# Performance work log

Hardware: AMD Instinct MI355X
Metric: run time of the kernel (lower is better)

The kernel has to match this reference:

```python
import jax, jax.numpy as jnp
import numpy as np

B, N, D = 4, 10000, 64
C, E = 2, 160000  # adj channels, edges per (graph, channel)
EPS = 1e-10


def setup_inputs() -> dict:
    key = jax.random.key(0)
    k1, k2, k3 = jax.random.split(key, 3)
    inputs = jax.random.normal(k1, (B, N, D), dtype=jnp.float32)
    edge_idx = jax.random.randint(k2, (B, C, E, 2), 0, N, dtype=jnp.int32)
    weight_a = 0.1 * jax.random.normal(k3, (C, 2 * D, 1), dtype=jnp.float32)
    return {"inputs": inputs, "edge_idx": edge_idx, "weight_a": weight_a}


def _gat_channel(x, idx, wa):
    # x: [N, D], idx: [E, 2] (col 0 = scatter/dst node, col 1 = gather/src node), wa: [2D, 1]
    n = x.shape[0]
    a1 = x[idx[:, 1]]                      # [E, D]
    a2 = x[idx[:, 0]]                      # [E, D]
    score = jnp.concatenate([a1, a2], axis=1) @ wa   # [E, 1]
    e = jnp.exp(jax.nn.leaky_relu(score, negative_slope=0.2))  # [E, 1]
    denom = jax.ops.segment_sum(e, idx[:, 0], num_segments=n)  # [N, 1]  (ii @ e)
    denom_e = denom[idx[:, 1]]             # [E, 1]  (faithful to original: gather by idx[:,1])
    alpha = e / (denom_e + EPS)            # [E, 1]
    r = jax.ops.segment_sum(alpha * a1, idx[:, 0], num_segments=n)  # [N, D]
    return jax.nn.sigmoid(r)


def _gat_graph(x, idx_all, weight_a):
    # x: [N, D], idx_all: [C, E, 2], weight_a: [C, 2D, 1]
    per_ch = jax.vmap(_gat_channel, in_axes=(None, 0, 0))(x, idx_all, weight_a)  # [C, N, D]
    return per_ch.sum(axis=0)


def reference(inputs, edge_idx, weight_a):
    # inputs: [B, N, D], edge_idx: [B, C, E, 2], weight_a: [C, 2D, 1]
    return jax.vmap(_gat_graph, in_axes=(0, 0, None))(inputs, edge_idx, weight_a)
```

## Files before the change

### kernel.cpp

```cpp
#include <hip/hip_runtime.h>

#define B_ 4
#define N_ 10000
#define D_ 64
#define C_ 2
#define E_ 160000
#define BC_ (B_ * C_)
#define G_ 40
#define CAP_ 5120
#define NBLK_ 25
#define EPB_ 6400
#define EPS_ 1e-10f

__global__ void gat_y(const float* __restrict__ x, const float* __restrict__ wa,
                      float* __restrict__ y1, float* __restrict__ y0) {
    int bc = blockIdx.x & 7;
    int n  = (blockIdx.x >> 3) * 256 + threadIdx.x;
    if (n >= N_) return;
    int b = bc / C_, c = bc % C_;
    const float4* xr = (const float4*)(x + ((size_t)b * N_ + n) * D_);
    const float4* w1 = (const float4*)(wa + (size_t)c * 2 * D_);
    const float4* w0 = w1 + D_ / 4;
    float a = 0.f, bb = 0.f;
#pragma unroll
    for (int i = 0; i < D_ / 4; ++i) {
        float4 xv = xr[i];
        float4 u = w1[i], v = w0[i];
        a  += xv.x * u.x + xv.y * u.y + xv.z * u.z + xv.w * u.w;
        bb += xv.x * v.x + xv.y * v.y + xv.z * v.z + xv.w * v.w;
    }
    y1[bc * N_ + n] = a;
    y0[bc * N_ + n] = bb;
}

__global__ void gat_bucket(const int* __restrict__ eidx, int* __restrict__ gcount,
                           unsigned int* __restrict__ bpack) {
    int bc  = blockIdx.x & 7;
    int blk = blockIdx.x >> 3;
    const int2* ep = (const int2*)eidx + (size_t)bc * E_ + (size_t)blk * EPB_;
    __shared__ int hist[G_];
    __shared__ int cur[G_];
    if (threadIdx.x < G_) hist[threadIdx.x] = 0;
    __syncthreads();
    int2 ev[25];
#pragma unroll
    for (int k = 0; k < 25; ++k) {
        ev[k] = ep[k * 256 + threadIdx.x];
        atomicAdd(&hist[ev[k].x >> 8], 1);
    }
    __syncthreads();
    if (threadIdx.x < G_)
        cur[threadIdx.x] = atomicAdd(&gcount[bc * G_ + threadIdx.x], hist[threadIdx.x]);
    __syncthreads();
    unsigned int base = (unsigned int)bc * G_ * CAP_;
#pragma unroll
    for (int k = 0; k < 25; ++k) {
        int g   = ev[k].x >> 8;
        int off = atomicAdd(&cur[g], 1);
        bpack[base + g * CAP_ + off] =
            ((unsigned int)(ev[k].x & 255) << 16) | (unsigned int)ev[k].y;
    }
}

__global__ void gat_fine(const unsigned int* __restrict__ bpack,
                         const int* __restrict__ gcount,
                         const float* __restrict__ y1, const float* __restrict__ y0,
                         unsigned short* __restrict__ csr_i1, float* __restrict__ csr_ee,
                         int* __restrict__ rs_s, int* __restrict__ rs_e,
                         float* __restrict__ rd) {
    int bc = blockIdx.x & 7;
    int g  = blockIdx.x >> 3;
    int K  = gcount[bc * G_ + g];
    int R  = bc * G_ * CAP_ + g * CAP_;
    const unsigned int* bp = bpack + R;
    const float* y1p = y1 + bc * N_;

    __shared__ int   cnt[256], excl[256], cur[256];
    __shared__ float y0l[256];
    __shared__ unsigned short li1[CAP_];
    __shared__ float lee[CAP_];
    __shared__ int sd[256];

    int node = g * 256 + threadIdx.x;
    cnt[threadIdx.x] = 0;
    y0l[threadIdx.x] = (node < N_) ? y0[bc * N_ + node] : 0.f;
    __syncthreads();

    for (int j = threadIdx.x; j < K; j += 256)
        atomicAdd(&cnt[bp[j] >> 16], 1);
    __syncthreads();

    int v = cnt[threadIdx.x];
    sd[threadIdx.x] = v;
    __syncthreads();
#pragma unroll
    for (int off = 1; off < 256; off <<= 1) {
        int t = (threadIdx.x >= off) ? sd[threadIdx.x - off] : 0;
        __syncthreads();
        sd[threadIdx.x] += t;
        __syncthreads();
    }
    int ex = sd[threadIdx.x] - v;
    excl[threadIdx.x] = ex;
    cur[threadIdx.x]  = ex;
    if (node < N_) {
        rs_s[bc * N_ + node] = R + ex;
        rs_e[bc * N_ + node] = R + ex + v;
    }
    __syncthreads();

    for (int j = threadIdx.x; j < K; j += 256) {
        unsigned int p = bp[j];
        int ln = p >> 16;
        int i1 = p & 0xffff;
        int slot = atomicAdd(&cur[ln], 1);
        li1[slot] = (unsigned short)i1;
        float sc = y1p[i1] + y0l[ln];
        lee[slot] = __expf(sc > 0.f ? sc : 0.2f * sc);
    }
    __syncthreads();

    if (node < N_) {
        int s = excl[threadIdx.x], t = s + v;
        float sum = 0.f;
        for (int j = s; j < t; ++j) sum += lee[j];
        rd[bc * N_ + node] = 1.f / (sum + EPS_);
    }
    for (int j = threadIdx.x; j < K; j += 256) {
        csr_i1[R + j] = li1[j];
        csr_ee[R + j] = lee[j];
    }
}

__global__ void gat_acc(const float* __restrict__ x, const int* __restrict__ rs_s,
                        const int* __restrict__ rs_e,
                        const unsigned short* __restrict__ csr_i1,
                        const float* __restrict__ csr_ee, const float* __restrict__ rd,
                        float* __restrict__ out) {
    int lane = threadIdx.x & 63;
    int w    = threadIdx.x >> 6;
    int b    = blockIdx.x & 3;
    int nn   = blockIdx.x >> 2;
    int n    = nn * 2 + (w >> 1);
    int c    = w & 1;
    int bc = b * C_ + c;
    const float* xb  = x + (size_t)b * N_ * D_ + lane;
    const float* rdp = rd + bc * N_;
    int s = rs_s[bc * N_ + n], t = rs_e[bc * N_ + n];
    float acc = 0.f;
    for (int base = s; base < t; base += 64) {
        int m = t - base; if (m > 64) m = 64;
        int a = 0; float wgt = 0.f;
        if (lane < m) {
            a   = csr_i1[base + lane];
            wgt = csr_ee[base + lane] * rdp[a];
        }
        int mp = (m + 3) & ~3;
        for (int j = 0; j < mp; j += 4) {
            int   a0 = __shfl(a, j),     a1 = __shfl(a, j + 1);
            int   a2 = __shfl(a, j + 2), a3 = __shfl(a, j + 3);
            float w0 = __shfl(wgt, j),     w1 = __shfl(wgt, j + 1);
            float w2 = __shfl(wgt, j + 2), w3 = __shfl(wgt, j + 3);
            float x0 = xb[a0 * D_], x1 = xb[a1 * D_];
            float x2 = xb[a2 * D_], x3 = xb[a3 * D_];
            acc += w0 * x0;
            acc += w1 * x1;
            acc += w2 * x2;
            acc += w3 * x3;
        }
    }
    float sg = 1.f / (1.f + __expf(-acc));
    __shared__ float sh[2][64];
    if (c == 1) sh[w >> 1][lane] = sg;
    __syncthreads();
    if (c == 0) out[((size_t)b * N_ + n) * D_ + lane] = sg + sh[w >> 1][lane];
}

extern "C" void kernel_launch(void* const* d_in, const int* in_sizes, int n_in,
                              void* d_out, int out_size, void* d_ws, size_t ws_size,
                              hipStream_t stream) {
    const float* x    = (const float*)d_in[0];
    const int*   eidx = (const int*)d_in[1];
    const float* wa   = (const float*)d_in[2];
    float* out = (float*)d_out;

    int*   gcount = (int*)d_ws;
    float* y1     = (float*)d_ws + 512;
    float* y0     = y1 + BC_ * N_;
    float* rd     = y0 + BC_ * N_;
    int*   rs_s   = (int*)(rd + BC_ * N_);
    int*   rs_e   = rs_s + BC_ * N_;
    unsigned int* bpack  = (unsigned int*)(rs_e + BC_ * N_);
    float*        csr_ee = (float*)(bpack + (size_t)BC_ * G_ * CAP_);
    unsigned short* csr_i1 = (unsigned short*)(csr_ee + (size_t)BC_ * G_ * CAP_);

    hipMemsetAsync(gcount, 0, BC_ * G_ * sizeof(int), stream);

    gat_y     <<<BC_ * 40,    256, 0, stream>>>(x, wa, y1, y0);
    gat_bucket<<<BC_ * NBLK_, 256, 0, stream>>>(eidx, gcount, bpack);
    gat_fine  <<<BC_ * G_,    256, 0, stream>>>(bpack, gcount, y1, y0,
                                                csr_i1, csr_ee, rs_s, rs_e, rd);
    gat_acc   <<<B_ * N_ / 2, 256, 0, stream>>>(x, rs_s, rs_e, csr_i1, csr_ee, rd, out);
}
```

Baseline: 142.8 us.

## Use finer node buckets and more bucketing blocks, unroll gather by eight

Shrinks the per-bucket node range from 256 to 128 nodes, which doubles the number of gat_fine blocks to 632, and splits edge bucketing across 125 blocks of 1280 edges instead of 25 blocks of 6400. The aim is more parallelism and better occupancy in the bucket and fine-CSR stages, plus less per-block serial work. The gather-accumulate loop is also unrolled from 4 to 8 to keep more loads in flight. The trade-off is more global atomics on bucket counters, half the threads idle in the fine stage's scan, and padded iterations when a node has few edges.

```diff
diff --git a/kernel.cpp b/kernel.cpp
--- a/kernel.cpp
+++ b/kernel.cpp
@@ -6,10 +6,13 @@
 #define C_ 2
 #define E_ 160000
 #define BC_ (B_ * C_)
-#define G_ 40
-#define CAP_ 5120
-#define NBLK_ 25
-#define EPB_ 6400
+#define SH2_ 7
+#define NB2_ 128
+#define G2_ 79
+#define CAPF_ 2560
+#define NBLK_ 125
+#define EPT_ 5
+#define EPB_ (256 * EPT_)
 #define EPS_ 1e-10f
 
 __global__ void gat_y(const float* __restrict__ x, const float* __restrict__ wa,
@@ -38,27 +41,26 @@
     int bc  = blockIdx.x & 7;
     int blk = blockIdx.x >> 3;
     const int2* ep = (const int2*)eidx + (size_t)bc * E_ + (size_t)blk * EPB_;
-    __shared__ int hist[G_];
-    __shared__ int cur[G_];
-    if (threadIdx.x < G_) hist[threadIdx.x] = 0;
-    __syncthreads();
-    int2 ev[25];
+    __shared__ int hist[G2_];
+    __shared__ int cur[G2_];
+    if (threadIdx.x < G2_) hist[threadIdx.x] = 0;
+    __syncthreads();
+    int2 ev[EPT_];
 #pragma unroll
-    for (int k = 0; k < 25; ++k) {
+    for (int k = 0; k < EPT_; ++k) {
         ev[k] = ep[k * 256 + threadIdx.x];
-        atomicAdd(&hist[ev[k].x >> 8], 1);
-    }
-    __syncthreads();
-    if (threadIdx.x < G_)
-        cur[threadIdx.x] = atomicAdd(&gcount[bc * G_ + threadIdx.x], hist[threadIdx.x]);
-    __syncthreads();
-    unsigned int base = (unsigned int)bc * G_ * CAP_;
+        atomicAdd(&hist[ev[k].x >> SH2_], 1);
+    }
+    __syncthreads();
+    if (threadIdx.x < G2_)
+        cur[threadIdx.x] = atomicAdd(&gcount[bc * G2_ + threadIdx.x], hist[threadIdx.x]);
+    __syncthreads();
 #pragma unroll
-    for (int k = 0; k < 25; ++k) {
-        int g   = ev[k].x >> 8;
+    for (int k = 0; k < EPT_; ++k) {
+        int g   = ev[k].x >> SH2_;
         int off = atomicAdd(&cur[g], 1);
-        bpack[base + g * CAP_ + off] =
-            ((unsigned int)(ev[k].x & 255) << 16) | (unsigned int)ev[k].y;
+        bpack[((size_t)bc * G2_ + g) * CAPF_ + off] =
+            ((unsigned int)(ev[k].x & (NB2_ - 1)) << 16) | (unsigned int)ev[k].y;
     }
 }
 
@@ -70,46 +72,49 @@
                          float* __restrict__ rd) {
     int bc = blockIdx.x & 7;
     int g  = blockIdx.x >> 3;
-    int K  = gcount[bc * G_ + g];
-    int R  = bc * G_ * CAP_ + g * CAP_;
+    int K  = gcount[bc * G2_ + g];
+    int R  = (bc * G2_ + g) * CAPF_;
     const unsigned int* bp = bpack + R;
     const float* y1p = y1 + bc * N_;
-
-    __shared__ int   cnt[256], excl[256], cur[256];
-    __shared__ float y0l[256];
-    __shared__ unsigned short li1[CAP_];
-    __shared__ float lee[CAP_];
-    __shared__ int sd[256];
-
-    int node = g * 256 + threadIdx.x;
-    cnt[threadIdx.x] = 0;
-    y0l[threadIdx.x] = (node < N_) ? y0[bc * N_ + node] : 0.f;
-    __syncthreads();
-
-    for (int j = threadIdx.x; j < K; j += 256)
+    int tid = threadIdx.x;
+
+    __shared__ int   cnt[NB2_], excl[NB2_], cur[NB2_], sd[NB2_];
+    __shared__ float y0l[NB2_];
+    __shared__ unsigned short li1[CAPF_];
+    __shared__ float lee[CAPF_];
+
+    int node = g * NB2_ + tid;
+    if (tid < NB2_) {
+        cnt[tid] = 0;
+        y0l[tid] = (node < N_) ? y0[bc * N_ + node] : 0.f;
+    }
+    __syncthreads();
+
+    for (int j = tid; j < K; j += 256)
         atomicAdd(&cnt[bp[j] >> 16], 1);
     __syncthreads();
 
-    int v = cnt[threadIdx.x];
-    sd[threadIdx.x] = v;
-    __syncthreads();
-#pragma unroll
-    for (int off = 1; off < 256; off <<= 1) {
-        int t = (threadIdx.x >= off) ? sd[threadIdx.x - off] : 0;
+    int v = 0;
+    if (tid < NB2_) { v = cnt[tid]; sd[tid] = v; }
+    __syncthreads();
+    for (int off = 1; off < NB2_; off <<= 1) {
+        int t = (tid < NB2_ && tid >= off) ? sd[tid - off] : 0;
         __syncthreads();
-        sd[threadIdx.x] += t;
+        if (tid < NB2_) sd[tid] += t;
         __syncthreads();
     }
-    int ex = sd[threadIdx.x] - v;
-    excl[threadIdx.x] = ex;
-    cur[threadIdx.x]  = ex;
-    if (node < N_) {
-        rs_s[bc * N_ + node] = R + ex;
-        rs_e[bc * N_ + node] = R + ex + v;
-    }
-    __syncthreads();
-
-    for (int j = threadIdx.x; j < K; j += 256) {
+    if (tid < NB2_) {
+        int ex = sd[tid] - v;
+        excl[tid] = ex;
+        cur[tid]  = ex;
+        if (node < N_) {
+            rs_s[bc * N_ + node] = R + ex;
+            rs_e[bc * N_ + node] = R + ex + v;
+        }
+    }
+    __syncthreads();
+
+    for (int j = tid; j < K; j += 256) {
         unsigned int p = bp[j];
         int ln = p >> 16;
         int i1 = p & 0xffff;
@@ -120,13 +125,13 @@
     }
     __syncthreads();
 
-    if (node < N_) {
-        int s = excl[threadIdx.x], t = s + v;
+    if (tid < NB2_ && node < N_) {
+        int s = excl[tid], t = s + v;
         float sum = 0.f;
         for (int j = s; j < t; ++j) sum += lee[j];
         rd[bc * N_ + node] = 1.f / (sum + EPS_);
     }
-    for (int j = threadIdx.x; j < K; j += 256) {
+    for (int j = tid; j < K; j += 256) {
         csr_i1[R + j] = li1[j];
         csr_ee[R + j] = lee[j];
     }
@@ -155,18 +160,28 @@
             a   = csr_i1[base + lane];
             wgt = csr_ee[base + lane] * rdp[a];
         }
-        int mp = (m + 3) & ~3;
-        for (int j = 0; j < mp; j += 4) {
+        int mp = (m + 7) & ~7;
+        for (int j = 0; j < mp; j += 8) {
             int   a0 = __shfl(a, j),     a1 = __shfl(a, j + 1);
             int   a2 = __shfl(a, j + 2), a3 = __shfl(a, j + 3);
+            int   a4 = __shfl(a, j + 4), a5 = __shfl(a, j + 5);
+            int   a6 = __shfl(a, j + 6), a7 = __shfl(a, j + 7);
             float w0 = __shfl(wgt, j),     w1 = __shfl(wgt, j + 1);
             float w2 = __shfl(wgt, j + 2), w3 = __shfl(wgt, j + 3);
+            float w4 = __shfl(wgt, j + 4), w5 = __shfl(wgt, j + 5);
+            float w6 = __shfl(wgt, j + 6), w7 = __shfl(wgt, j + 7);
             float x0 = xb[a0 * D_], x1 = xb[a1 * D_];
             float x2 = xb[a2 * D_], x3 = xb[a3 * D_];
+            float x4 = xb[a4 * D_], x5 = xb[a5 * D_];
+            float x6 = xb[a6 * D_], x7 = xb[a7 * D_];
             acc += w0 * x0;
             acc += w1 * x1;
             acc += w2 * x2;
             acc += w3 * x3;
+            acc += w4 * x4;
+            acc += w5 * x5;
+            acc += w6 * x6;
+            acc += w7 * x7;
         }
     }
     float sg = 1.f / (1.f + __expf(-acc));
@@ -185,20 +200,20 @@
     float* out = (float*)d_out;
 
     int*   gcount = (int*)d_ws;
-    float* y1     = (float*)d_ws + 512;
+    float* y1     = (float*)d_ws + 1024;
     float* y0     = y1 + BC_ * N_;
     float* rd     = y0 + BC_ * N_;
     int*   rs_s   = (int*)(rd + BC_ * N_);
     int*   rs_e   = rs_s + BC_ * N_;
     unsigned int* bpack  = (unsigned int*)(rs_e + BC_ * N_);
-    float*        csr_ee = (float*)(bpack + (size_t)BC_ * G_ * CAP_);
-    unsigned short* csr_i1 = (unsigned short*)(csr_ee + (size_t)BC_ * G_ * CAP_);
-
-    hipMemsetAsync(gcount, 0, BC_ * G_ * sizeof(int), stream);
+    float*        csr_ee = (float*)(bpack + (size_t)BC_ * G2_ * CAPF_);
+    unsigned short* csr_i1 = (unsigned short*)(csr_ee + (size_t)BC_ * G2_ * CAPF_);
+
+    hipMemsetAsync(gcount, 0, BC_ * G2_ * sizeof(int), stream);
 
     gat_y     <<<BC_ * 40,    256, 0, stream>>>(x, wa, y1, y0);
     gat_bucket<<<BC_ * NBLK_, 256, 0, stream>>>(eidx, gcount, bpack);
-    gat_fine  <<<BC_ * G_,    256, 0, stream>>>(bpack, gcount, y1, y0,
+    gat_fine  <<<BC_ * G2_,   256, 0, stream>>>(bpack, gcount, y1, y0,
                                                 csr_i1, csr_ee, rs_s, rs_e, rd);
     gat_acc   <<<B_ * N_ / 2, 256, 0, stream>>>(x, rs_s, rs_e, csr_i1, csr_ee, rd, out);
 }
```

Measured after the change: 137.8 us. 1.04x faster.
